# Performance work log

Measured on AMD Instinct MI355X. Metric: run time of the kernel, lower is better.

The kernel has to match this reference:

```python
import jax, jax.numpy as jnp
import numpy as np

BS, N = 32, 512
NHALF = N // 2            # mapped atoms per sample (half reactant, half product)
IN_X, IN_E, IN_C, IN_BD = 16, 5, 3, 3
OUT_X, OUT_E, OUT_C, OUT_BD = 16, 5, 3, 3


def setup_inputs() -> dict:
    key = jax.random.key(0)
    k = jax.random.split(key, 6)
    X = jax.random.normal(k[0], (BS, N, IN_X), dtype=jnp.float32)
    E = jax.random.normal(k[1], (BS, N, N, IN_E), dtype=jnp.float32)
    atom_charges = jax.random.normal(k[2], (BS, N, IN_C), dtype=jnp.float32)
    bond_dirs = jax.random.normal(k[3], (BS, N, N, IN_BD), dtype=jnp.float32)
    # atom map numbers: reactant half and product half each carry a permutation of 1..NHALF
    rk = jax.random.split(k[4], BS)
    pk = jax.random.split(k[5], BS)
    rct_amn = jax.vmap(lambda kk: jax.random.permutation(kk, NHALF))(rk).astype(jnp.int32) + 1
    prod_amn = jax.vmap(lambda kk: jax.random.permutation(kk, NHALF))(pk).astype(jnp.int32) + 1
    atom_map_numbers = jnp.concatenate([rct_amn, prod_amn], axis=1)  # [BS,N]
    mol_assignment = jnp.concatenate([
        jnp.ones((BS, NHALF), jnp.int32),       # reactant atoms
        jnp.full((BS, NHALF), 2, jnp.int32),    # product atoms (max assignment)
    ], axis=1)
    return {"X": X, "E": E, "atom_charges": atom_charges, "bond_dirs": bond_dirs,
            "atom_map_numbers": atom_map_numbers, "mol_assignment": mol_assignment}


def _alignment_maps(atom_map_numbers, mol_assignment):
    """Vectorized equivalent of the per-sample python loops: for each reactant
    position j with atom-map number m>0 (present among product atoms), find the
    product position carrying the same m ('correct' alignment_type)."""
    bs, n = atom_map_numbers.shape
    bidx = jnp.arange(bs)[:, None]
    prod_assign = mol_assignment.max(axis=-1, keepdims=True)
    amn_prod = jnp.where(mol_assignment == prod_assign, atom_map_numbers, 0)  # [bs,n]
    amn_rct = jnp.where(mol_assignment < prod_assign, atom_map_numbers, 0)
    # rowwise_atom_mapping_mask: keep only rct numbers present in prod row
    present = jnp.zeros((bs, n + 1), bool).at[bidx, amn_prod].set(True)
    present = present.at[:, 0].set(False)
    amn_rct = jnp.where(jnp.take_along_axis(present, amn_rct, axis=1), amn_rct, 0)
    # inverse table: prodpos_table[i,m] = product position j with amn_prod[i,j]==m
    pos = jnp.broadcast_to(jnp.arange(n, dtype=jnp.int32), (bs, n))
    prodpos_table = jnp.zeros((bs, n + 1), jnp.int32).at[bidx, amn_prod].set(pos)
    prodpos = jnp.take_along_axis(prodpos_table, amn_rct, axis=1)  # [bs,n]
    mask = amn_rct > 0  # reactant positions that received aligned product features
    return prodpos, mask


def _gather_pairs(T, p):
    # T: [bs,n,n,d], p: [bs,n] -> T[i, p[j1], p[j2], :]
    return jax.vmap(lambda Ti, pi: Ti[pi][:, pi])(T, p)


def reference(X, E, atom_charges, bond_dirs, atom_map_numbers, mol_assignment):
    prodpos, mask = _alignment_maps(atom_map_numbers, mol_assignment)
    m1 = mask[..., None].astype(X.dtype)
    pair = (mask[:, :, None] & mask[:, None, :])  # [bs,n,n]
    pairf = pair[..., None].astype(X.dtype)

    # node-feature alignment (gather product features, scatter to reactant slots)
    Xg = jnp.take_along_axis(X[..., :OUT_X], prodpos[..., None], axis=1) * m1
    Cg = jnp.take_along_axis(atom_charges[..., :OUT_C], prodpos[..., None], axis=1) * m1

    # edge-feature alignment
    E1 = _gather_pairs(E[..., :OUT_E], prodpos) * pairf          # aligned product edges
    onehot0 = jax.nn.one_hot(0, E.shape[-1], dtype=X.dtype)
    E2 = (1.0 - pairf) * onehot0                                  # skip conn on non-mapped pairs
    BD1 = _gather_pairs(bond_dirs[..., :OUT_BD], prodpos) * pairf

    X_cat = jnp.concatenate([X, Xg], axis=-1)
    C_cat = jnp.concatenate([atom_charges, Cg], axis=-1)
    return (X_cat, C_cat, E1, E2, BD1)
```

## Files before the change

kernel.cpp:

```cpp
#include <hip/hip_runtime.h>
#include <hip/hip_bf16.h>

#define BSZ 32
#define NN  512

static const long O_XC = 0;
static const long O_CC = 524288L;
static const long O_E1 = 622592L;
static const long O_E2 = 42565632L;
static const long O_BD = 84508672L;

typedef float f32x4 __attribute__((ext_vector_type(4)));

__global__ __launch_bounds__(NN) void align_kernel(
    const int* __restrict__ amn, const int* __restrict__ ma,
    int* __restrict__ p2m)
{
    const int i = blockIdx.x;
    const int t = threadIdx.x;

    __shared__ int red[NN];
    __shared__ int table[NN + 1];

    const int a = ma[i * NN + t];
    red[t] = a;
    __syncthreads();
    for (int s = NN / 2; s > 0; s >>= 1) {
        if (t < s) red[t] = max(red[t], red[t + s]);
        __syncthreads();
    }
    const int prod_assign = red[0];

    table[t] = -1;
    if (t == 0) table[NN] = -1;
    __syncthreads();

    const int m = amn[i * NN + t];
    if (a == prod_assign && m > 0 && m <= NN) table[m] = t;
    __syncthreads();

    int p = -1;
    if (a < prod_assign && m > 0 && m <= NN) p = table[m];
    p2m[i * NN + t] = p;
}

__global__ __launch_bounds__(256) void node_kernel(
    const float* __restrict__ X,
    const float* __restrict__ AC,
    const int* __restrict__ p2m,
    float* __restrict__ out)
{
    const int idx = blockIdx.x * 256 + threadIdx.x;
    if (idx >= BSZ * NN) return;
    const int i = idx >> 9;
    const int p = p2m[idx];

    const float4* xr4 = (const float4*)(X + (size_t)idx * 16);
    float4* ox4 = (float4*)(out + O_XC + (size_t)idx * 32);
#pragma unroll
    for (int c = 0; c < 4; ++c) ox4[c] = xr4[c];
    if (p >= 0) {
        const float4* xp4 = (const float4*)(X + ((size_t)i * NN + p) * 16);
#pragma unroll
        for (int c = 0; c < 4; ++c) ox4[4 + c] = xp4[c];
    } else {
        const float4 z = make_float4(0.f, 0.f, 0.f, 0.f);
#pragma unroll
        for (int c = 0; c < 4; ++c) ox4[4 + c] = z;
    }

    const float* cr = AC + (size_t)idx * 3;
    float* oc = out + O_CC + (size_t)idx * 6;
#pragma unroll
    for (int c = 0; c < 3; ++c) oc[c] = cr[c];
    if (p >= 0) {
        const float* cp = AC + ((size_t)i * NN + p) * 3;
#pragma unroll
        for (int c = 0; c < 3; ++c) oc[3 + c] = cp[c];
    } else {
#pragma unroll
        for (int c = 0; c < 3; ++c) oc[3 + c] = 0.0f;
    }
}

__global__ __launch_bounds__(NN) void edge_kernel(
    const float* __restrict__ E,
    const float* __restrict__ BD,
    const int* __restrict__ p2m,
    float* __restrict__ out)
{
    const int b  = blockIdx.x;
    const int i  = b >> 9;
    const int j1 = b & (NN - 1);
    const int t  = threadIdx.x;

    f32x4* oE1 = (f32x4*)(out + O_E1 + (size_t)b * (NN * 5));
    f32x4* oE2 = (f32x4*)(out + O_E2 + (size_t)b * (NN * 5));
    f32x4* oBD = (f32x4*)(out + O_BD + (size_t)b * (NN * 3));

    __shared__ int   sp[NN];
    __shared__ float sE[NN * 5];
    __shared__ float sB[NN * 3];

    const int p1 = p2m[i * NN + j1];

    if (p1 < 0) {
        const f32x4 z = {0.f, 0.f, 0.f, 0.f};
        for (int f = t; f < 640; f += NN) {
            f32x4 v2;
#pragma unroll
            for (int k = 0; k < 4; ++k) {
                const int g  = 4 * f + k;
                const int j2 = g / 5;
                const int c  = g - j2 * 5;
                v2[k] = (c == 0) ? 1.0f : 0.0f;
            }
            __builtin_nontemporal_store(z,  oE1 + f);
            __builtin_nontemporal_store(v2, oE2 + f);
        }
        for (int f = t; f < 384; f += NN)
            __builtin_nontemporal_store(z, oBD + f);
        return;
    }

    sp[t] = p2m[i * NN + t];
    {
        const f32x4* Er4 = (const f32x4*)(E  + ((size_t)i * NN + p1) * (NN * 5));
        const f32x4* Br4 = (const f32x4*)(BD + ((size_t)i * NN + p1) * (NN * 3));
        f32x4* sE4 = (f32x4*)sE;
        f32x4* sB4 = (f32x4*)sB;
        sE4[t] = Er4[t];
        if (t < 128) sE4[NN + t] = Er4[NN + t];
        if (t < 384) sB4[t] = Br4[t];
    }
    __syncthreads();

    for (int f = t; f < 640; f += NN) {
        f32x4 v1, v2;
#pragma unroll
        for (int k = 0; k < 4; ++k) {
            const int g   = 4 * f + k;
            const int j2  = g / 5;
            const int c   = g - j2 * 5;
            const int p2  = sp[j2];
            const int p2c = p2 < 0 ? 0 : p2;
            const float e = sE[p2c * 5 + c];
            const bool pair = (p2 >= 0);
            v1[k] = pair ? e : 0.0f;
            v2[k] = pair ? 0.0f : (c == 0 ? 1.0f : 0.0f);
        }
        __builtin_nontemporal_store(v1, oE1 + f);
        __builtin_nontemporal_store(v2, oE2 + f);
    }

    for (int f = t; f < 384; f += NN) {
        f32x4 v;
#pragma unroll
        for (int k = 0; k < 4; ++k) {
            const int g   = 4 * f + k;
            const int j2  = g / 3;
            const int c   = g - j2 * 3;
            const int p2  = sp[j2];
            const int p2c = p2 < 0 ? 0 : p2;
            const float x = sB[p2c * 3 + c];
            v[k] = (p2 >= 0) ? x : 0.0f;
        }
        __builtin_nontemporal_store(v, oBD + f);
    }
}

extern "C" void kernel_launch(void* const* d_in, const int* in_sizes, int n_in,
                              void* d_out, int out_size, void* d_ws, size_t ws_size,
                              hipStream_t stream) {
    const float* X  = (const float*)d_in[0];
    const float* E  = (const float*)d_in[1];
    const float* AC = (const float*)d_in[2];
    const float* BD = (const float*)d_in[3];
    const int* amn = (const int*)d_in[4];
    const int* ma  = (const int*)d_in[5];
    float* out = (float*)d_out;

    int* p2m = (int*)d_ws;

    align_kernel<<<BSZ, NN, 0, stream>>>(amn, ma, p2m);
    node_kernel<<<(BSZ * NN + 255) / 256, 256, 0, stream>>>(X, AC, p2m, out);
    edge_kernel<<<BSZ * NN, NN, 0, stream>>>(E, BD, p2m, out);
}
```

Measured before the change: 594.2 us.

## Split fused edge kernel into separate E1, E2 and BD kernels with 256 threads

The single edge kernel that wrote E1, E2 and bond-direction outputs per row is split into three kernels, each with 256-thread blocks and smaller shared-memory footprints. E2 no longer needs any input row from E, only the mapping table. Nontemporal stores are replaced with regular stores. The aim is higher occupancy and simpler per-kernel streams, at the cost of two extra launches and reloading the mapping row three times.

Result: no change. 588.0 us (-1.0%).

```diff
diff --git a/kernel.cpp b/kernel.cpp
--- a/kernel.cpp
+++ b/kernel.cpp
@@ -83,60 +83,38 @@
     }
 }
 
-__global__ __launch_bounds__(NN) void edge_kernel(
+
+__global__ __launch_bounds__(256) void e1_kernel(
     const float* __restrict__ E,
-    const float* __restrict__ BD,
-    const int* __restrict__ p2m,
-    float* __restrict__ out)
-{
-    const int b  = blockIdx.x;
-    const int i  = b >> 9;
-    const int j1 = b & (NN - 1);
-    const int t  = threadIdx.x;
-
-    f32x4* oE1 = (f32x4*)(out + O_E1 + (size_t)b * (NN * 5));
-    f32x4* oE2 = (f32x4*)(out + O_E2 + (size_t)b * (NN * 5));
-    f32x4* oBD = (f32x4*)(out + O_BD + (size_t)b * (NN * 3));
+    const int* __restrict__ p2m,
+    float* __restrict__ out)
+{
+    const int b = blockIdx.x;
+    const int i = b >> 9;
+    const int t = threadIdx.x;
+
+    f32x4* o = (f32x4*)(out + O_E1 + (size_t)b * (NN * 5));
+    const int p1 = p2m[b];
+
+    if (p1 < 0) {
+        const f32x4 z = {0.f, 0.f, 0.f, 0.f};
+        for (int f = t; f < 640; f += 256) o[f] = z;
+        return;
+    }
 
     __shared__ int   sp[NN];
     __shared__ float sE[NN * 5];
-    __shared__ float sB[NN * 3];
-
-    const int p1 = p2m[i * NN + j1];
-
-    if (p1 < 0) {
-        const f32x4 z = {0.f, 0.f, 0.f, 0.f};
-        for (int f = t; f < 640; f += NN) {
-            f32x4 v2;
-#pragma unroll
-            for (int k = 0; k < 4; ++k) {
-                const int g  = 4 * f + k;
-                const int j2 = g / 5;
-                const int c  = g - j2 * 5;
-                v2[k] = (c == 0) ? 1.0f : 0.0f;
-            }
-            __builtin_nontemporal_store(z,  oE1 + f);
-            __builtin_nontemporal_store(v2, oE2 + f);
-        }
-        for (int f = t; f < 384; f += NN)
-            __builtin_nontemporal_store(z, oBD + f);
-        return;
-    }
-
-    sp[t] = p2m[i * NN + t];
+    sp[t]       = p2m[i * NN + t];
+    sp[t + 256] = p2m[i * NN + t + 256];
     {
-        const f32x4* Er4 = (const f32x4*)(E  + ((size_t)i * NN + p1) * (NN * 5));
-        const f32x4* Br4 = (const f32x4*)(BD + ((size_t)i * NN + p1) * (NN * 3));
+        const f32x4* Er4 = (const f32x4*)(E + ((size_t)i * NN + p1) * (NN * 5));
         f32x4* sE4 = (f32x4*)sE;
-        f32x4* sB4 = (f32x4*)sB;
-        sE4[t] = Er4[t];
-        if (t < 128) sE4[NN + t] = Er4[NN + t];
-        if (t < 384) sB4[t] = Br4[t];
-    }
-    __syncthreads();
-
-    for (int f = t; f < 640; f += NN) {
-        f32x4 v1, v2;
+        for (int f = t; f < 640; f += 256) sE4[f] = Er4[f];
+    }
+    __syncthreads();
+
+    for (int f = t; f < 640; f += 256) {
+        f32x4 v;
 #pragma unroll
         for (int k = 0; k < 4; ++k) {
             const int g   = 4 * f + k;
@@ -145,15 +123,86 @@
             const int p2  = sp[j2];
             const int p2c = p2 < 0 ? 0 : p2;
             const float e = sE[p2c * 5 + c];
-            const bool pair = (p2 >= 0);
-            v1[k] = pair ? e : 0.0f;
-            v2[k] = pair ? 0.0f : (c == 0 ? 1.0f : 0.0f);
-        }
-        __builtin_nontemporal_store(v1, oE1 + f);
-        __builtin_nontemporal_store(v2, oE2 + f);
-    }
-
-    for (int f = t; f < 384; f += NN) {
+            v[k] = (p2 >= 0) ? e : 0.0f;
+        }
+        o[f] = v;
+    }
+}
+
+__global__ __launch_bounds__(256) void e2_kernel(
+    const int* __restrict__ p2m,
+    float* __restrict__ out)
+{
+    const int b = blockIdx.x;
+    const int i = b >> 9;
+    const int t = threadIdx.x;
+
+    f32x4* o = (f32x4*)(out + O_E2 + (size_t)b * (NN * 5));
+    const int p1 = p2m[b];
+
+    if (p1 < 0) {
+        for (int f = t; f < 640; f += 256) {
+            f32x4 v;
+#pragma unroll
+            for (int k = 0; k < 4; ++k) {
+                const int g  = 4 * f + k;
+                const int j2 = g / 5;
+                const int c  = g - j2 * 5;
+                v[k] = (c == 0) ? 1.0f : 0.0f;
+            }
+            o[f] = v;
+        }
+        return;
+    }
+
+    __shared__ int sp[NN];
+    sp[t]       = p2m[i * NN + t];
+    sp[t + 256] = p2m[i * NN + t + 256];
+    __syncthreads();
+
+    for (int f = t; f < 640; f += 256) {
+        f32x4 v;
+#pragma unroll
+        for (int k = 0; k < 4; ++k) {
+            const int g  = 4 * f + k;
+            const int j2 = g / 5;
+            const int c  = g - j2 * 5;
+            v[k] = (sp[j2] >= 0) ? 0.0f : (c == 0 ? 1.0f : 0.0f);
+        }
+        o[f] = v;
+    }
+}
+
+__global__ __launch_bounds__(256) void bd_kernel(
+    const float* __restrict__ BD,
+    const int* __restrict__ p2m,
+    float* __restrict__ out)
+{
+    const int b = blockIdx.x;
+    const int i = b >> 9;
+    const int t = threadIdx.x;
+
+    f32x4* o = (f32x4*)(out + O_BD + (size_t)b * (NN * 3));
+    const int p1 = p2m[b];
+
+    if (p1 < 0) {
+        const f32x4 z = {0.f, 0.f, 0.f, 0.f};
+        for (int f = t; f < 384; f += 256) o[f] = z;
+        return;
+    }
+
+    __shared__ int   sp[NN];
+    __shared__ float sB[NN * 3];
+    sp[t]       = p2m[i * NN + t];
+    sp[t + 256] = p2m[i * NN + t + 256];
+    {
+        const f32x4* Br4 = (const f32x4*)(BD + ((size_t)i * NN + p1) * (NN * 3));
+        f32x4* sB4 = (f32x4*)sB;
+        for (int f = t; f < 384; f += 256) sB4[f] = Br4[f];
+    }
+    __syncthreads();
+
+    for (int f = t; f < 384; f += 256) {
         f32x4 v;
 #pragma unroll
         for (int k = 0; k < 4; ++k) {
@@ -165,7 +214,7 @@
             const float x = sB[p2c * 3 + c];
             v[k] = (p2 >= 0) ? x : 0.0f;
         }
-        __builtin_nontemporal_store(v, oBD + f);
+        o[f] = v;
     }
 }
 
@@ -184,5 +233,7 @@
 
     align_kernel<<<BSZ, NN, 0, stream>>>(amn, ma, p2m);
     node_kernel<<<(BSZ * NN + 255) / 256, 256, 0, stream>>>(X, AC, p2m, out);
-    edge_kernel<<<BSZ * NN, NN, 0, stream>>>(E, BD, p2m, out);
-}
+    e1_kernel<<<BSZ * NN, 256, 0, stream>>>(E, p2m, out);
+    e2_kernel<<<BSZ * NN, 256, 0, stream>>>(p2m, out);
+    bd_kernel<<<BSZ * NN, 256, 0, stream>>>(BD, p2m, out);
+}
```

## Fuse node and edge kernels, process eight rows per block with direct gathers

Applied to the files above, without the earlier changes.

Merges the node and edge kernels into one launch in which each 256-thread block handles eight j1 rows of a sample. The p2m row is loaded into shared memory once per block and reused across all eight rows. The shared-memory staging of each E/BD row is dropped in favour of direct gathered global loads, and nontemporal stores become ordinary stores. This saves a launch and repeated index loads, but the global reads are now uncoalesced gathers and the outputs may pollute the cache.

Result: no change. 603.5 us (+1.6%).

```diff
diff --git a/kernel.cpp b/kernel.cpp
--- a/kernel.cpp
+++ b/kernel.cpp
@@ -3,6 +3,7 @@
 
 #define BSZ 32
 #define NN  512
+#define G   8
 
 static const long O_XC = 0;
 static const long O_CC = 524288L;
@@ -44,128 +45,135 @@
     p2m[i * NN + t] = p;
 }
 
-__global__ __launch_bounds__(256) void node_kernel(
+__global__ __launch_bounds__(256) void fused_kernel(
     const float* __restrict__ X,
+    const float* __restrict__ E,
     const float* __restrict__ AC,
-    const int* __restrict__ p2m,
-    float* __restrict__ out)
-{
-    const int idx = blockIdx.x * 256 + threadIdx.x;
-    if (idx >= BSZ * NN) return;
-    const int i = idx >> 9;
-    const int p = p2m[idx];
-
-    const float4* xr4 = (const float4*)(X + (size_t)idx * 16);
-    float4* ox4 = (float4*)(out + O_XC + (size_t)idx * 32);
-#pragma unroll
-    for (int c = 0; c < 4; ++c) ox4[c] = xr4[c];
-    if (p >= 0) {
-        const float4* xp4 = (const float4*)(X + ((size_t)i * NN + p) * 16);
-#pragma unroll
-        for (int c = 0; c < 4; ++c) ox4[4 + c] = xp4[c];
-    } else {
-        const float4 z = make_float4(0.f, 0.f, 0.f, 0.f);
-#pragma unroll
-        for (int c = 0; c < 4; ++c) ox4[4 + c] = z;
-    }
-
-    const float* cr = AC + (size_t)idx * 3;
-    float* oc = out + O_CC + (size_t)idx * 6;
-#pragma unroll
-    for (int c = 0; c < 3; ++c) oc[c] = cr[c];
-    if (p >= 0) {
-        const float* cp = AC + ((size_t)i * NN + p) * 3;
-#pragma unroll
-        for (int c = 0; c < 3; ++c) oc[3 + c] = cp[c];
-    } else {
-#pragma unroll
-        for (int c = 0; c < 3; ++c) oc[3 + c] = 0.0f;
-    }
-}
-
-__global__ __launch_bounds__(NN) void edge_kernel(
-    const float* __restrict__ E,
     const float* __restrict__ BD,
     const int* __restrict__ p2m,
     float* __restrict__ out)
 {
-    const int b  = blockIdx.x;
-    const int i  = b >> 9;
-    const int j1 = b & (NN - 1);
-    const int t  = threadIdx.x;
+    const int blk = blockIdx.x;
+    const int i   = blk >> 6;
+    const int j0  = (blk & 63) * G;
+    const int t   = threadIdx.x;
 
-    f32x4* oE1 = (f32x4*)(out + O_E1 + (size_t)b * (NN * 5));
-    f32x4* oE2 = (f32x4*)(out + O_E2 + (size_t)b * (NN * 5));
-    f32x4* oBD = (f32x4*)(out + O_BD + (size_t)b * (NN * 3));
+    __shared__ int sp[NN];
+    sp[t]       = p2m[i * NN + t];
+    sp[t + 256] = p2m[i * NN + t + 256];
+    __syncthreads();
 
-    __shared__ int   sp[NN];
-    __shared__ float sE[NN * 5];
-    __shared__ float sB[NN * 3];
-
-    const int p1 = p2m[i * NN + j1];
-
-    if (p1 < 0) {
-        const f32x4 z = {0.f, 0.f, 0.f, 0.f};
-        for (int f = t; f < 640; f += NN) {
-            f32x4 v2;
+    if (t < G * 8) {
+        const int r = t >> 3, q = t & 7;
+        const int j1 = j0 + r;
+        const size_t idx = (size_t)i * NN + j1;
+        const int p = sp[j1];
+        float4 v = make_float4(0.f, 0.f, 0.f, 0.f);
+        if (q < 4) {
+            v = ((const float4*)(X + idx * 16))[q];
+        } else if (p >= 0) {
+            v = ((const float4*)(X + ((size_t)i * NN + p) * 16))[q - 4];
+        }
+        ((float4*)(out + O_XC + idx * 32))[q] = v;
+    } else if (t < G * 8 + G * 2) {
+        const int u = t - G * 8;
+        const int r = u >> 1, h = u & 1;
+        const int j1 = j0 + r;
+        const size_t idx = (size_t)i * NN + j1;
+        const int p = sp[j1];
+        float* dst = out + O_CC + idx * 6 + h * 3;
+        if (h == 0) {
+            const float* src = AC + idx * 3;
 #pragma unroll
-            for (int k = 0; k < 4; ++k) {
-                const int g  = 4 * f + k;
-                const int j2 = g / 5;
-                const int c  = g - j2 * 5;
-                v2[k] = (c == 0) ? 1.0f : 0.0f;
-            }
-            __builtin_nontemporal_store(z,  oE1 + f);
-            __builtin_nontemporal_store(v2, oE2 + f);
+            for (int c = 0; c < 3; ++c) dst[c] = src[c];
+        } else if (p >= 0) {
+            const float* src = AC + ((size_t)i * NN + p) * 3;
+#pragma unroll
+            for (int c = 0; c < 3; ++c) dst[c] = src[c];
+        } else {
+#pragma unroll
+            for (int c = 0; c < 3; ++c) dst[c] = 0.0f;
         }
-        for (int f = t; f < 384; f += NN)
-            __builtin_nontemporal_store(z, oBD + f);
-        return;
     }
 
-    sp[t] = p2m[i * NN + t];
-    {
-        const f32x4* Er4 = (const f32x4*)(E  + ((size_t)i * NN + p1) * (NN * 5));
-        const f32x4* Br4 = (const f32x4*)(BD + ((size_t)i * NN + p1) * (NN * 3));
-        f32x4* sE4 = (f32x4*)sE;
-        f32x4* sB4 = (f32x4*)sB;
-        sE4[t] = Er4[t];
-        if (t < 128) sE4[NN + t] = Er4[NN + t];
-        if (t < 384) sB4[t] = Br4[t];
-    }
-    __syncthreads();
+    for (int r = 0; r < G; ++r) {
+        const int j1 = j0 + r;
+        const size_t b = (size_t)i * NN + j1;
+        const int p1 = sp[j1];
 
-    for (int f = t; f < 640; f += NN) {
-        f32x4 v1, v2;
+        f32x4* oE1 = (f32x4*)(out + O_E1 + b * (NN * 5));
+        f32x4* oE2 = (f32x4*)(out + O_E2 + b * (NN * 5));
+        f32x4* oBD = (f32x4*)(out + O_BD + b * (NN * 3));
+
+        if (p1 < 0) {
+            const f32x4 z = {0.f, 0.f, 0.f, 0.f};
 #pragma unroll
-        for (int k = 0; k < 4; ++k) {
-            const int g   = 4 * f + k;
-            const int j2  = g / 5;
-            const int c   = g - j2 * 5;
-            const int p2  = sp[j2];
-            const int p2c = p2 < 0 ? 0 : p2;
-            const float e = sE[p2c * 5 + c];
-            const bool pair = (p2 >= 0);
-            v1[k] = pair ? e : 0.0f;
-            v2[k] = pair ? 0.0f : (c == 0 ? 1.0f : 0.0f);
+            for (int u = 0; u < 3; ++u) {
+                const int f = t + u * 256;
+                if (u < 2 || t < 128) {
+                    f32x4 v2;
+#pragma unroll
+                    for (int k = 0; k < 4; ++k) {
+                        const int g  = 4 * f + k;
+                        const int j2 = g / 5;
+                        const int c  = g - j2 * 5;
+                        v2[k] = (c == 0) ? 1.0f : 0.0f;
+                    }
+                    oE1[f] = z;
+                    oE2[f] = v2;
+                }
+            }
+#pragma unroll
+            for (int u = 0; u < 2; ++u) {
+                const int f = t + u * 256;
+                if (u < 1 || t < 128) oBD[f] = z;
+            }
+            continue;
         }
-        __builtin_nontemporal_store(v1, oE1 + f);
-        __builtin_nontemporal_store(v2, oE2 + f);
-    }
 
-    for (int f = t; f < 384; f += NN) {
-        f32x4 v;
+        const float* __restrict__ Erow = E  + ((size_t)i * NN + p1) * (NN * 5);
+        const float* __restrict__ Brow = BD + ((size_t)i * NN + p1) * (NN * 3);
+
 #pragma unroll
-        for (int k = 0; k < 4; ++k) {
-            const int g   = 4 * f + k;
-            const int j2  = g / 3;
-            const int c   = g - j2 * 3;
-            const int p2  = sp[j2];
-            const int p2c = p2 < 0 ? 0 : p2;
-            const float x = sB[p2c * 3 + c];
-            v[k] = (p2 >= 0) ? x : 0.0f;
+        for (int u = 0; u < 3; ++u) {
+            const int f = t + u * 256;
+            if (u < 2 || t < 128) {
+                f32x4 v1, v2;
+#pragma unroll
+                for (int k = 0; k < 4; ++k) {
+                    const int g   = 4 * f + k;
+                    const int j2  = g / 5;
+                    const int c   = g - j2 * 5;
+                    const int p2  = sp[j2];
+                    const int p2c = p2 < 0 ? 0 : p2;
+                    const float e = Erow[p2c * 5 + c];
+                    const bool pair = (p2 >= 0);
+                    v1[k] = pair ? e : 0.0f;
+                    v2[k] = pair ? 0.0f : (c == 0 ? 1.0f : 0.0f);
+                }
+                oE1[f] = v1;
+                oE2[f] = v2;
+            }
         }
-        __builtin_nontemporal_store(v, oBD + f);
+
+#pragma unroll
+        for (int u = 0; u < 2; ++u) {
+            const int f = t + u * 256;
+            if (u < 1 || t < 128) {
+                f32x4 v;
+#pragma unroll
+                for (int k = 0; k < 4; ++k) {
+                    const int g   = 4 * f + k;
+                    const int j2  = g / 3;
+                    const int c   = g - j2 * 3;
+                    const int p2  = sp[j2];
+                    const int p2c = p2 < 0 ? 0 : p2;
+                    const float x = Brow[p2c * 3 + c];
+                    v[k] = (p2 >= 0) ? x : 0.0f;
+                }
+                oBD[f] = v;
+            }
+        }
     }
 }
 
@@ -183,6 +191,5 @@
     int* p2m = (int*)d_ws;
 
     align_kernel<<<BSZ, NN, 0, stream>>>(amn, ma, p2m);
-    node_kernel<<<(BSZ * NN + 255) / 256, 256, 0, stream>>>(X, AC, p2m, out);
-    edge_kernel<<<BSZ * NN, NN, 0, stream>>>(E, BD, p2m, out);
+    fused_kernel<<<(BSZ * NN) / G, 256, 0, stream>>>(X, E, AC, BD, p2m, out);
 }
```
